# Kernel tuning notes

Hardware: AMD Instinct MI355X
Metric: run time of the kernel (lower is better)

Reference implementation:

```python
import jax, jax.numpy as jnp
import numpy as np

N_NODES = 100000
N_EDGES = 1600000
IN_DIM, HID_DIM, OUT_DIM = 256, 64, 64


def gcn_conv(x, src, dst, W, b, n_nodes):
    """PyG GCNConv: D^-1/2 (A + I) D^-1/2 X W + b (self-loops added, deg on dst)."""
    h = x @ W  # [N, D_out]
    ones = jnp.ones(src.shape[0], dtype=h.dtype)
    deg = jax.ops.segment_sum(ones, dst, num_segments=n_nodes) + 1.0  # +1 for self-loop
    dinv = jax.lax.rsqrt(deg)  # deg >= 1, always finite
    norm = dinv[src] * dinv[dst]  # [E]
    # neighbor aggregation (scatter-add) + self-loop contribution
    agg = jax.ops.segment_sum(h[src] * norm[:, None], dst, num_segments=n_nodes)
    agg = agg + h * (dinv * dinv)[:, None]
    return agg + b


def gcn_backbone(x, edge_index, W1, b1, W2, b2, n_nodes):
    src, dst = edge_index[0], edge_index[1]
    h = jax.nn.relu(gcn_conv(x, src, dst, W1, b1, n_nodes))
    h = gcn_conv(h, src, dst, W2, b2, n_nodes)
    return h


def zscore(h):
    # torch .std(0) is unbiased (ddof=1)
    return (h - h.mean(axis=0)) / jnp.std(h, axis=0, ddof=1)


def setup_inputs() -> dict:
    key = jax.random.key(0)
    k = jax.random.split(key, 8)
    x1 = jax.random.normal(k[0], (N_NODES, IN_DIM), dtype=jnp.float32)
    x2 = jax.random.normal(k[1], (N_NODES, IN_DIM), dtype=jnp.float32)
    edge_index1 = jax.random.randint(k[2], (2, N_EDGES), 0, N_NODES, dtype=jnp.int64)
    edge_index2 = jax.random.randint(k[3], (2, N_EDGES), 0, N_NODES, dtype=jnp.int64)
    W1 = jax.random.normal(k[4], (IN_DIM, HID_DIM), dtype=jnp.float32) * (1.0 / np.sqrt(IN_DIM))
    b1 = jnp.zeros((HID_DIM,), dtype=jnp.float32)
    W2 = jax.random.normal(k[5], (HID_DIM, OUT_DIM), dtype=jnp.float32) * (1.0 / np.sqrt(HID_DIM))
    b2 = jnp.zeros((OUT_DIM,), dtype=jnp.float32)
    return {"x1": x1, "edge_index1": edge_index1, "x2": x2, "edge_index2": edge_index2,
            "W1": W1, "b1": b1, "W2": W2, "b2": b2}


def reference(x1, edge_index1, x2, edge_index2, W1, b1, W2, b2):
    h1 = gcn_backbone(x1, edge_index1, W1, b1, W2, b2, N_NODES)
    h2 = gcn_backbone(x2, edge_index2, W1, b1, W2, b2, N_NODES)
    return zscore(h1), zscore(h2)
```

## Files before the change

### kernel.cpp

```cpp
#include <hip/hip_runtime.h>
#include <hip/hip_bf16.h>

#define HD 64
#define CH 8192
#define BKT_SHIFT 10
#define SRC_BITS 17
#define MAXBLK 256

typedef __attribute__((ext_vector_type(8))) short bf16x8;
typedef __attribute__((ext_vector_type(4))) float f32x4;

typedef __attribute__((address_space(1))) const unsigned int* gas_ptr;
typedef __attribute__((address_space(3))) unsigned int* las_ptr;

__device__ inline void gl_lds16(const void* g, void* l) {
  __builtin_amdgcn_global_load_lds((gas_ptr)g, (las_ptr)l, 16, 0, 0);
}

__device__ inline unsigned short f2bf(float x) {
  unsigned u = __float_as_uint(x);
  unsigned r = u + 0x7FFF + ((u >> 16) & 1);
  return (unsigned short)(r >> 16);
}
__device__ inline float bf2f(unsigned short h) {
  return __uint_as_float(((unsigned)h) << 16);
}

__global__ __launch_bounds__(256) void k_wprep(const float* __restrict__ W1,
                                               const float* __restrict__ W2,
                                               unsigned short* __restrict__ Wf1,
                                               unsigned short* __restrict__ Wf2hi,
                                               unsigned short* __restrict__ Wf2lo) {
  int idx = blockIdx.x * blockDim.x + threadIdx.x;
  if (idx < 256 * 64) {
    int k = idx >> 6, c = idx & 63;
    float w = W1[idx];
    int ks = k >> 5, r = k & 31, h2 = r >> 3, j = r & 7;
    int f = c >> 4, r16c = c & 15;
    int pos = (((ks * 4 + f) * 64) + h2 * 16 + r16c) * 8 + j;
    Wf1[pos] = f2bf(w);
  } else if (idx < 256 * 64 + 64 * 64) {
    int i2 = idx - 256 * 64;
    int k = i2 >> 6, c = i2 & 63;
    float w = W2[i2];
    int ks = k >> 5, r = k & 31, h2 = r >> 3, j = r & 7;
    int f = c >> 4, r16c = c & 15;
    int pos = (((ks * 4 + f) * 64) + h2 * 16 + r16c) * 8 + j;
    unsigned short hi = f2bf(w);
    Wf2hi[pos] = hi;
    Wf2lo[pos] = f2bf(w - bf2f(hi));
  }
}

__global__ __launch_bounds__(256) void k_bin1(const int* __restrict__ src0,
                                              const int* __restrict__ dst0,
                                              const int* __restrict__ src1,
                                              const int* __restrict__ dst1,
                                              int* __restrict__ tmp,
                                              int* __restrict__ counts,
                                              int* __restrict__ offsets,
                                              int NB, int NBLK, int E) {
  __shared__ int hist[128];
  __shared__ int pref[128];
  __shared__ int lofs[128];
  __shared__ int stage[CH];
  const int g = blockIdx.x / NBLK;
  const int blk = blockIdx.x % NBLK;
  const int* __restrict__ src = g ? src1 : src0;
  const int* __restrict__ dst = g ? dst1 : dst0;
  int* __restrict__ tmpg = tmp + (size_t)g * NBLK * CH;
  int* __restrict__ cntg = counts + (size_t)g * NB * NBLK;
  int* __restrict__ offg = offsets + (size_t)g * NB * NBLK;
  const int e0 = blk * CH;
  const int len = min(CH, E - e0);
  const int t = threadIdx.x;

  for (int i = t; i < 128; i += 256) hist[i] = 0;
  __syncthreads();
  int dreg[CH / 256];
#pragma unroll
  for (int it = 0; it < CH / 256; ++it) {
    int i = t + it * 256;
    if (i < len) {
      int d = dst[e0 + i];
      dreg[it] = d;
      atomicAdd(&hist[d >> BKT_SHIFT], 1);
    }
  }
  __syncthreads();
  if (t < 128) pref[t] = hist[t];
  __syncthreads();
  for (int off = 1; off < 128; off <<= 1) {
    int v = 0;
    if (t < 128 && t >= off) v = pref[t - off];
    __syncthreads();
    if (t < 128) pref[t] += v;
    __syncthreads();
  }
  if (t < NB) {
    int ex = pref[t] - hist[t];
    lofs[t] = ex;
    cntg[t * NBLK + blk] = hist[t];
    offg[t * NBLK + blk] = ex;
  }
  __syncthreads();
#pragma unroll
  for (int it = 0; it < CH / 256; ++it) {
    int i = t + it * 256;
    if (i < len) {
      int d = dreg[it], s = src[e0 + i];
      int slot = atomicAdd(&lofs[d >> BKT_SHIFT], 1);
      stage[slot] = ((d & ((1 << BKT_SHIFT) - 1)) << SRC_BITS) | s;
    }
  }
  __syncthreads();
  int nv = len >> 2;
  for (int i = t; i < nv; i += 256) ((int4*)(tmpg + e0))[i] = ((const int4*)stage)[i];
  for (int i = (nv << 2) + t; i < len; i += 256) tmpg[e0 + i] = stage[i];
}

__global__ __launch_bounds__(128) void k_bscan(const int* __restrict__ counts,
                                               int* __restrict__ bucket_base,
                                               int* __restrict__ row_start,
                                               int NB, int NBLK, int N, int E) {
  __shared__ int sh[128];
  const int g = blockIdx.x;
  const int* __restrict__ cntg = counts + (size_t)g * NB * NBLK;
  int* __restrict__ bbg = bucket_base + g * (NB + 1);
  int* __restrict__ rsg = row_start + (size_t)g * (N + 1);
  int t = threadIdx.x;
  int v = 0;
  if (t < NB) {
    const int* p = cntg + t * NBLK;
    for (int i = 0; i < NBLK; ++i) v += p[i];
  }
  sh[t] = v;
  __syncthreads();
  for (int off = 1; off < 128; off <<= 1) {
    int x = (t >= off) ? sh[t - off] : 0;
    __syncthreads();
    sh[t] += x;
    __syncthreads();
  }
  if (t < NB) bbg[t] = sh[t] - v;
  if (t == 0) {
    bbg[NB] = E;
    rsg[N] = E;
  }
}

__global__ __launch_bounds__(1024) void k_bin2m(const int* __restrict__ tmp,
                                                const int* __restrict__ counts,
                                                const int* __restrict__ offsets,
                                                const int* __restrict__ bucket_base,
                                                int* __restrict__ row_start,
                                                float* __restrict__ dinv,
                                                int* __restrict__ recs, int N, int NB,
                                                int NBLK, int E) {
  __shared__ int h[1 << BKT_SHIFT];
  __shared__ int lcur[1 << BKT_SHIFT];
  __shared__ int scnt[MAXBLK], soff[MAXBLK];
  const int g = blockIdx.x / NB;
  const int b = blockIdx.x % NB;
  const int* __restrict__ tmpg = tmp + (size_t)g * NBLK * CH;
  const int* __restrict__ cntg = counts + (size_t)g * NB * NBLK;
  const int* __restrict__ offg = offsets + (size_t)g * NB * NBLK;
  const int* __restrict__ bbg = bucket_base + g * (NB + 1);
  int* __restrict__ rsg = row_start + (size_t)g * (N + 1);
  float* __restrict__ dig = dinv + (size_t)g * N;
  int* __restrict__ recg = recs + (size_t)g * E;
  const int t = threadIdx.x;
  const int node0 = b << BKT_SHIFT;
  const int lane = t & 63, w = t >> 6;

  h[t] = 0;
  for (int i = t; i < NBLK; i += 1024) {
    scnt[i] = cntg[b * NBLK + i];
    soff[i] = offg[b * NBLK + i];
  }
  __syncthreads();
  for (int blk = w; blk < NBLK; blk += 16) {
    int cnt = scnt[blk];
    const int* p = tmpg + blk * CH + soff[blk];
    for (int j = lane; j < cnt; j += 64) atomicAdd(&h[p[j] >> SRC_BITS], 1);
  }
  __syncthreads();
  int deg = h[t];
  __syncthreads();
  for (int off = 1; off < 1024; off <<= 1) {
    int x = (t >= off) ? h[t - off] : 0;
    __syncthreads();
    h[t] += x;
    __syncthreads();
  }
  int base = bbg[b] + h[t] - deg;
  lcur[t] = base;
  int n = node0 + t;
  if (n < N) {
    rsg[n] = base;
    dig[n] = rsqrtf((float)deg + 1.0f);
  }
  __syncthreads();
  for (int blk = w; blk < NBLK; blk += 16) {
    int cnt = scnt[blk];
    const int* p = tmpg + blk * CH + soff[blk];
    for (int j = lane; j < cnt; j += 64) {
      int rec = p[j];
      int d = rec >> SRC_BITS;
      int s = rec & ((1 << SRC_BITS) - 1);
      int slot = atomicAdd(&lcur[d], 1);
      recg[slot] = s;
    }
  }
}

__global__ __launch_bounds__(256) void k_gemm1(const float* __restrict__ X0,
                                               const float* __restrict__ X1,
                                               const unsigned short* __restrict__ Wf1,
                                               unsigned short* __restrict__ Hb, int N,
                                               int gPer) {
  __shared__ float sA[2][64 * 64];
  const int tid = threadIdx.x;
  const int g = blockIdx.x / gPer;
  const int bblk = blockIdx.x % gPer;
  const float* __restrict__ Xv = g ? X1 : X0;
  const int row0 = bblk * 64;
  const int lane = tid & 63;
  const int wv = tid >> 6;
  const int r16 = lane & 15;
  const int half = lane >> 4;
  const int rowL = wv * 16 + r16;

  auto STAGE = [&](int b, int c) {
#pragma unroll
    for (int i = 0; i < 4; ++i) {
      int slot = tid + i * 256;
      int r = slot >> 4, u = slot & 15;
      int su = (u & 8) | ((u & 7) ^ (r & 7));
      int gr = min(row0 + r, N - 1);
      gl_lds16(Xv + (size_t)gr * 256 + c * 64 + su * 4, (char*)&sA[b][0] + slot * 16);
    }
  };

  f32x4 acc[4];
#pragma unroll
  for (int f = 0; f < 4; ++f) acc[f] = (f32x4){0.f, 0.f, 0.f, 0.f};

  STAGE(0, 0);
  for (int c = 0; c < 4; ++c) {
    const int buf = c & 1;
    if (c < 3) STAGE(buf ^ 1, c + 1);
    __syncthreads();
#pragma unroll
    for (int ks2 = 0; ks2 < 2; ++ks2) {
      const int ksg = c * 2 + ks2;
      int v0 = ks2 * 8 + half * 2;
      int p0 = (v0 & 8) | ((v0 & 7) ^ (rowL & 7));
      int p1 = ((v0 + 1) & 8) | (((v0 + 1) & 7) ^ (rowL & 7));
      float4 a0 = *(const float4*)((const char*)&sA[buf][0] + (rowL * 16 + p0) * 16);
      float4 a1 = *(const float4*)((const char*)&sA[buf][0] + (rowL * 16 + p1) * 16);
      union { __hip_bfloat162 h[4]; bf16x8 v; } cu;
      cu.h[0] = __float22bfloat162_rn(make_float2(a0.x, a0.y));
      cu.h[1] = __float22bfloat162_rn(make_float2(a0.z, a0.w));
      cu.h[2] = __float22bfloat162_rn(make_float2(a1.x, a1.y));
      cu.h[3] = __float22bfloat162_rn(make_float2(a1.z, a1.w));
      bf16x8 ahi = cu.v;
#pragma unroll
      for (int f = 0; f < 4; ++f) {
        bf16x8 bh = *(const bf16x8*)&Wf1[(((ksg * 4 + f) * 64) + lane) * 8];
        acc[f] = __builtin_amdgcn_mfma_f32_16x16x32_bf16(ahi, bh, acc[f], 0, 0, 0);
      }
    }
    __syncthreads();
  }

  const int orow0 = row0 + wv * 16 + half * 4;
#pragma unroll
  for (int f = 0; f < 4; ++f) {
#pragma unroll
    for (int rg = 0; rg < 4; ++rg) {
      int orow = orow0 + rg;
      if (orow < N) Hb[((size_t)g * N + orow) * HD + f * 16 + r16] = f2bf(acc[f][rg]);
    }
  }
}

__global__ __launch_bounds__(256) void k_gemm2(const unsigned short* __restrict__ Xb,
                                               const unsigned short* __restrict__ Wfh,
                                               const unsigned short* __restrict__ Wfl,
                                               unsigned short* __restrict__ Hb, int M) {
  __shared__ unsigned short sA[64 * 64];
  const int tid = threadIdx.x;
  const int row0 = blockIdx.x * 64;
  const int lane = tid & 63;
  const int wv = tid >> 6;
  const int r16 = lane & 15;
  const int half = lane >> 4;
  const int rowL = wv * 16 + r16;

#pragma unroll
  for (int i = 0; i < 2; ++i) {
    int slot = tid + i * 256;
    int r = slot >> 3, u = slot & 7;
    int su = u ^ (r & 7);
    int gr = min(row0 + r, M - 1);
    gl_lds16(Xb + (size_t)gr * 64 + su * 8, (char*)sA + slot * 16);
  }
  __syncthreads();

  f32x4 acc[4];
#pragma unroll
  for (int f = 0; f < 4; ++f) acc[f] = (f32x4){0.f, 0.f, 0.f, 0.f};

#pragma unroll
  for (int ks = 0; ks < 2; ++ks) {
    int v = ks * 4 + half;
    int p = v ^ (rowL & 7);
    bf16x8 ahi = *(const bf16x8*)((const char*)sA + (rowL * 8 + p) * 16);
#pragma unroll
    for (int f = 0; f < 4; ++f) {
      bf16x8 bh = *(const bf16x8*)&Wfh[(((ks * 4 + f) * 64) + lane) * 8];
      bf16x8 bl = *(const bf16x8*)&Wfl[(((ks * 4 + f) * 64) + lane) * 8];
      acc[f] = __builtin_amdgcn_mfma_f32_16x16x32_bf16(ahi, bh, acc[f], 0, 0, 0);
      acc[f] = __builtin_amdgcn_mfma_f32_16x16x32_bf16(ahi, bl, acc[f], 0, 0, 0);
    }
  }

  const int orow0 = row0 + wv * 16 + half * 4;
#pragma unroll
  for (int f = 0; f < 4; ++f) {
#pragma unroll
    for (int rg = 0; rg < 4; ++rg) {
      int orow = orow0 + rg;
      if (orow < M) Hb[(size_t)orow * HD + f * 16 + r16] = f2bf(acc[f][rg]);
    }
  }
}

template <int OUTBF16>
__global__ __launch_bounds__(256) void k_agg(const unsigned short* __restrict__ Hb,
                                             const int* __restrict__ recs,
                                             const int* __restrict__ row_start,
                                             const float* __restrict__ dinv,
                                             const float* __restrict__ bias,
                                             void* __restrict__ outv, int N, int E,
                                             int relu) {
  const int t = threadIdx.x;
  const int nglob = (blockIdx.x * blockDim.x + t) >> 4;
  const int lane16 = t & 15;
  if (nglob >= 2 * N) return;
  const int g = nglob >= N;
  const int node = nglob - g * N;
  const int* __restrict__ rsg = row_start + (size_t)g * (N + 1);
  const int* __restrict__ R = recs + (size_t)g * E;
  const float* __restrict__ dig = dinv + (size_t)g * N;
  const unsigned short* __restrict__ Hbg = Hb + (size_t)g * N * HD;

  const int c0 = lane16 * 4;
  float di = dig[node];
  float a0, a1, a2, a3;
  {
    uint2 h = *(const uint2*)&Hbg[(size_t)node * HD + c0];
    float dd = di * di;
    a0 = bf2f((unsigned short)(h.x & 0xffff)) * dd;
    a1 = bf2f((unsigned short)(h.x >> 16)) * dd;
    a2 = bf2f((unsigned short)(h.y & 0xffff)) * dd;
    a3 = bf2f((unsigned short)(h.y >> 16)) * dd;
  }
  const int beg = rsg[node], end = rsg[node + 1];
  int e = beg;
  for (; e + 8 <= end; e += 8) {
    int s[8];
    uint2 gg[8];
    float n[8];
#pragma unroll
    for (int j = 0; j < 8; ++j) s[j] = R[e + j];
#pragma unroll
    for (int j = 0; j < 8; ++j) {
      gg[j] = *(const uint2*)&Hbg[(size_t)s[j] * HD + c0];
      n[j] = dig[s[j]];
    }
#pragma unroll
    for (int j = 0; j < 8; ++j) {
      float nn = n[j] * di;
      a0 = fmaf(bf2f((unsigned short)(gg[j].x & 0xffff)), nn, a0);
      a1 = fmaf(bf2f((unsigned short)(gg[j].x >> 16)), nn, a1);
      a2 = fmaf(bf2f((unsigned short)(gg[j].y & 0xffff)), nn, a2);
      a3 = fmaf(bf2f((unsigned short)(gg[j].y >> 16)), nn, a3);
    }
  }
  for (; e < end; ++e) {
    int s = R[e];
    uint2 gg = *(const uint2*)&Hbg[(size_t)s * HD + c0];
    float nn = dig[s] * di;
    a0 = fmaf(bf2f((unsigned short)(gg.x & 0xffff)), nn, a0);
    a1 = fmaf(bf2f((unsigned short)(gg.x >> 16)), nn, a1);
    a2 = fmaf(bf2f((unsigned short)(gg.y & 0xffff)), nn, a2);
    a3 = fmaf(bf2f((unsigned short)(gg.y >> 16)), nn, a3);
  }
  float4 bv = *(const float4*)&bias[c0];
  a0 += bv.x; a1 += bv.y; a2 += bv.z; a3 += bv.w;
  if (relu) {
    a0 = fmaxf(a0, 0.f); a1 = fmaxf(a1, 0.f);
    a2 = fmaxf(a2, 0.f); a3 = fmaxf(a3, 0.f);
  }
  if (OUTBF16) {
    uint2 o;
    o.x = ((unsigned)f2bf(a1) << 16) | f2bf(a0);
    o.y = ((unsigned)f2bf(a3) << 16) | f2bf(a2);
    *(uint2*)&((unsigned short*)outv)[(size_t)nglob * HD + c0] = o;
  } else {
    *(float4*)&((float*)outv)[(size_t)nglob * HD + c0] = make_float4(a0, a1, a2, a3);
  }
}


__global__ void k_colstats(const float* __restrict__ H, float* __restrict__ stats, int N,
                           int gridPer) {
  __shared__ float ss[256], sq[256];
  const int g = blockIdx.x / gridPer;
  const int blk = blockIdx.x % gridPer;
  const float* __restrict__ Hg = H + (size_t)g * N * HD;
  float* __restrict__ st = stats + g * 128;
  int t = threadIdx.x;
  int col = t & 63, grp = t >> 6;
  float s = 0.f, q = 0.f;
  for (int row = blk * 4 + grp; row < N; row += gridPer * 4) {
    float v = Hg[(size_t)row * HD + col];
    s += v;
    q += v * v;
  }
  ss[t] = s;
  sq[t] = q;
  __syncthreads();
  if (t < 64) {
    s = ss[t] + ss[t + 64] + ss[t + 128] + ss[t + 192];
    q = sq[t] + sq[t + 64] + sq[t + 128] + sq[t + 192];
    atomicAdd(&st[t], s);
    atomicAdd(&st[64 + t], q);
  }
}

__global__ void k_normalize(float* __restrict__ H, const float* __restrict__ stats, int N) {
  int i = blockIdx.x * blockDim.x + threadIdx.x;
  int total = 2 * N * HD;
  if (i >= total) return;
  int col = i & 63;
  const float* st = stats + (i >= N * HD ? 128 : 0);
  float sum = st[col], sumsq = st[64 + col];
  float mean = sum / (float)N;
  float var = (sumsq - sum * sum / (float)N) / (float)(N - 1);
  float r = rsqrtf(var);
  H[i] = (H[i] - mean) * r;
}


extern "C" void kernel_launch(void* const* d_in, const int* in_sizes, int n_in,
                              void* d_out, int out_size, void* d_ws, size_t ws_size,
                              hipStream_t stream) {
  const int IN_DIM = 256;
  const float* X1 = (const float*)d_in[0];
  const float* X2 = (const float*)d_in[2];
  const int* EI1 = (const int*)d_in[1];
  const int* EI2 = (const int*)d_in[3];
  const float* W1 = (const float*)d_in[4];
  const float* b1 = (const float*)d_in[5];
  const float* W2 = (const float*)d_in[6];
  const float* b2 = (const float*)d_in[7];
  const int N = in_sizes[0] / IN_DIM;
  const int E = in_sizes[1] / 2;
  const int NB = (N + (1 << BKT_SHIFT) - 1) >> BKT_SHIFT;
  const int NBLK = (E + CH - 1) / CH;

  char* ws = (char*)d_ws;
  size_t off = 0;
  auto carve = [&](size_t bytes) -> char* {
    char* p = ws + off;
    off += (bytes + 255) & ~(size_t)255;
    return p;
  };
  unsigned short* Hb = (unsigned short*)carve((size_t)2 * N * HD * 2);
  int* tmp = (int*)carve((size_t)2 * NBLK * CH * 4);
  int* recs = (int*)carve((size_t)2 * E * 4);
  char* zero_base = carve(256 * 4);
  float* stats = (float*)zero_base;
  int* row_start = (int*)carve((size_t)2 * (N + 1) * 4);
  float* dinv = (float*)carve((size_t)2 * N * 4);
  int* bucket_base = (int*)carve((size_t)2 * (NB + 1) * 4);
  int* counts = (int*)carve((size_t)2 * NB * NBLK * 4);
  int* offsets = (int*)carve((size_t)2 * NB * NBLK * 4);
  unsigned short* Wf1 = (unsigned short*)carve(256 * 64 * 2);
  unsigned short* Wf2hi = (unsigned short*)carve(64 * 64 * 2);
  unsigned short* Wf2lo = (unsigned short*)carve(64 * 64 * 2);
  unsigned short* bufAgg = (unsigned short*)d_out;
  (void)ws_size; (void)n_in; (void)out_size;

  const int T = 256;
  const int gPer1 = (N + 63) / 64;
  const int gG2 = (2 * N + 63) / 64;
  const int gAgg = (2 * N * 16 + T - 1) / T;
  const int gCS = 512;
  const int gElem = (2 * N * HD + T - 1) / T;
  const int gWp = (256 * 64 + 64 * 64 + T - 1) / T;

  (void)hipMemsetAsync(zero_base, 0, 256 * 4, stream);
  k_wprep<<<gWp, T, 0, stream>>>(W1, W2, Wf1, Wf2hi, Wf2lo);
  k_bin1<<<2 * NBLK, T, 0, stream>>>(EI1, EI1 + E, EI2, EI2 + E, tmp, counts, offsets,
                                     NB, NBLK, E);
  k_bscan<<<2, 128, 0, stream>>>(counts, bucket_base, row_start, NB, NBLK, N, E);
  k_bin2m<<<2 * NB, 1024, 0, stream>>>(tmp, counts, offsets, bucket_base, row_start,
                                       dinv, recs, N, NB, NBLK, E);

  k_gemm1<<<2 * gPer1, T, 0, stream>>>(X1, X2, Wf1, Hb, N, gPer1);
  k_agg<1><<<gAgg, T, 0, stream>>>(Hb, recs, row_start, dinv, b1, bufAgg, N, E, 1);
  k_gemm2<<<gG2, T, 0, stream>>>(bufAgg, Wf2hi, Wf2lo, Hb, 2 * N);
  k_agg<0><<<gAgg, T, 0, stream>>>(Hb, recs, row_start, dinv, b2, d_out, N, E, 0);

  k_colstats<<<2 * gCS, T, 0, stream>>>((float*)d_out, stats, N, gCS);
  k_normalize<<<gElem, T, 0, stream>>>((float*)d_out, stats, N);
}
```

Before: 363.9 us.

## Load GEMM operands directly into registers via inline asm, dropping LDS staging

Both dense GEMM kernels stop staging the activation tile through shared memory with global_load_lds and barriers. Each lane now issues its own dwordx4 global loads straight into registers from inline assembly, covering its A-fragment rows and all the weight fragments, then waits with explicit vmcnt waits. In gemm1 the second half of the weights is loaded while the first half of the MFMAs runs. This removes LDS traffic and __syncthreads, but raises register pressure (many vector registers held per lane) and bypasses the compiler's own scheduling of the loads.

```diff
diff --git a/kernel.cpp b/kernel.cpp
--- a/kernel.cpp
+++ b/kernel.cpp
@@ -9,13 +9,10 @@
 
 typedef __attribute__((ext_vector_type(8))) short bf16x8;
 typedef __attribute__((ext_vector_type(4))) float f32x4;
-
-typedef __attribute__((address_space(1))) const unsigned int* gas_ptr;
-typedef __attribute__((address_space(3))) unsigned int* las_ptr;
-
-__device__ inline void gl_lds16(const void* g, void* l) {
-  __builtin_amdgcn_global_load_lds((gas_ptr)g, (las_ptr)l, 16, 0, 0);
-}
+typedef __attribute__((ext_vector_type(4))) unsigned int u32x4;
+
+#define WAITALL do { asm volatile("s_waitcnt vmcnt(0)" ::: "memory"); \
+                     __builtin_amdgcn_sched_barrier(0); } while (0)
 
 __device__ inline unsigned short f2bf(float x) {
   unsigned u = __float_as_uint(x);
@@ -219,62 +216,124 @@
                                                const unsigned short* __restrict__ Wf1,
                                                unsigned short* __restrict__ Hb, int N,
                                                int gPer) {
-  __shared__ float sA[2][64 * 64];
   const int tid = threadIdx.x;
   const int g = blockIdx.x / gPer;
   const int bblk = blockIdx.x % gPer;
   const float* __restrict__ Xv = g ? X1 : X0;
-  const int row0 = bblk * 64;
   const int lane = tid & 63;
   const int wv = tid >> 6;
   const int r16 = lane & 15;
   const int half = lane >> 4;
-  const int rowL = wv * 16 + r16;
-
-  auto STAGE = [&](int b, int c) {
-#pragma unroll
-    for (int i = 0; i < 4; ++i) {
-      int slot = tid + i * 256;
-      int r = slot >> 4, u = slot & 15;
-      int su = (u & 8) | ((u & 7) ^ (r & 7));
-      int gr = min(row0 + r, N - 1);
-      gl_lds16(Xv + (size_t)gr * 256 + c * 64 + su * 4, (char*)&sA[b][0] + slot * 16);
-    }
-  };
+  const int row = bblk * 64 + wv * 16 + r16;
+  const int rowc = min(row, N - 1);
+
+  unsigned long long xa =
+      (unsigned long long)(const void*)(Xv + (size_t)rowc * 256 + half * 8);
+  f32x4 a[16];
+  asm volatile(
+      "global_load_dwordx4 %0, %16, off\n\t"
+      "global_load_dwordx4 %1, %16, off offset:16\n\t"
+      "global_load_dwordx4 %2, %16, off offset:128\n\t"
+      "global_load_dwordx4 %3, %16, off offset:144\n\t"
+      "global_load_dwordx4 %4, %16, off offset:256\n\t"
+      "global_load_dwordx4 %5, %16, off offset:272\n\t"
+      "global_load_dwordx4 %6, %16, off offset:384\n\t"
+      "global_load_dwordx4 %7, %16, off offset:400\n\t"
+      "global_load_dwordx4 %8, %16, off offset:512\n\t"
+      "global_load_dwordx4 %9, %16, off offset:528\n\t"
+      "global_load_dwordx4 %10, %16, off offset:640\n\t"
+      "global_load_dwordx4 %11, %16, off offset:656\n\t"
+      "global_load_dwordx4 %12, %16, off offset:768\n\t"
+      "global_load_dwordx4 %13, %16, off offset:784\n\t"
+      "global_load_dwordx4 %14, %16, off offset:896\n\t"
+      "global_load_dwordx4 %15, %16, off offset:912\n\t"
+      : "=&v"(a[0]), "=&v"(a[1]), "=&v"(a[2]), "=&v"(a[3]), "=&v"(a[4]),
+        "=&v"(a[5]), "=&v"(a[6]), "=&v"(a[7]), "=&v"(a[8]), "=&v"(a[9]),
+        "=&v"(a[10]), "=&v"(a[11]), "=&v"(a[12]), "=&v"(a[13]), "=&v"(a[14]),
+        "=&v"(a[15])
+      : "v"(xa));
+
+  const unsigned long long wb = (unsigned long long)(const void*)Wf1 + lane * 16;
+  bf16x8 B[32];
+  asm volatile(
+      "global_load_dwordx4 %0, %16, off\n\t"
+      "global_load_dwordx4 %1, %16, off offset:1024\n\t"
+      "global_load_dwordx4 %2, %16, off offset:2048\n\t"
+      "global_load_dwordx4 %3, %16, off offset:3072\n\t"
+      "global_load_dwordx4 %4, %17, off\n\t"
+      "global_load_dwordx4 %5, %17, off offset:1024\n\t"
+      "global_load_dwordx4 %6, %17, off offset:2048\n\t"
+      "global_load_dwordx4 %7, %17, off offset:3072\n\t"
+      "global_load_dwordx4 %8, %18, off\n\t"
+      "global_load_dwordx4 %9, %18, off offset:1024\n\t"
+      "global_load_dwordx4 %10, %18, off offset:2048\n\t"
+      "global_load_dwordx4 %11, %18, off offset:3072\n\t"
+      "global_load_dwordx4 %12, %19, off\n\t"
+      "global_load_dwordx4 %13, %19, off offset:1024\n\t"
+      "global_load_dwordx4 %14, %19, off offset:2048\n\t"
+      "global_load_dwordx4 %15, %19, off offset:3072\n\t"
+      : "=&v"(B[0]), "=&v"(B[1]), "=&v"(B[2]), "=&v"(B[3]), "=&v"(B[4]),
+        "=&v"(B[5]), "=&v"(B[6]), "=&v"(B[7]), "=&v"(B[8]), "=&v"(B[9]),
+        "=&v"(B[10]), "=&v"(B[11]), "=&v"(B[12]), "=&v"(B[13]), "=&v"(B[14]),
+        "=&v"(B[15])
+      : "v"(wb), "v"(wb + 4096), "v"(wb + 8192), "v"(wb + 12288));
+
+  WAITALL;
+
+  asm volatile(
+      "global_load_dwordx4 %0, %16, off\n\t"
+      "global_load_dwordx4 %1, %16, off offset:1024\n\t"
+      "global_load_dwordx4 %2, %16, off offset:2048\n\t"
+      "global_load_dwordx4 %3, %16, off offset:3072\n\t"
+      "global_load_dwordx4 %4, %17, off\n\t"
+      "global_load_dwordx4 %5, %17, off offset:1024\n\t"
+      "global_load_dwordx4 %6, %17, off offset:2048\n\t"
+      "global_load_dwordx4 %7, %17, off offset:3072\n\t"
+      "global_load_dwordx4 %8, %18, off\n\t"
+      "global_load_dwordx4 %9, %18, off offset:1024\n\t"
+      "global_load_dwordx4 %10, %18, off offset:2048\n\t"
+      "global_load_dwordx4 %11, %18, off offset:3072\n\t"
+      "global_load_dwordx4 %12, %19, off\n\t"
+      "global_load_dwordx4 %13, %19, off offset:1024\n\t"
+      "global_load_dwordx4 %14, %19, off offset:2048\n\t"
+      "global_load_dwordx4 %15, %19, off offset:3072\n\t"
+      : "=&v"(B[16]), "=&v"(B[17]), "=&v"(B[18]), "=&v"(B[19]), "=&v"(B[20]),
+        "=&v"(B[21]), "=&v"(B[22]), "=&v"(B[23]), "=&v"(B[24]), "=&v"(B[25]),
+        "=&v"(B[26]), "=&v"(B[27]), "=&v"(B[28]), "=&v"(B[29]), "=&v"(B[30]),
+        "=&v"(B[31])
+      : "v"(wb + 16384), "v"(wb + 20480), "v"(wb + 24576), "v"(wb + 28672));
 
   f32x4 acc[4];
 #pragma unroll
   for (int f = 0; f < 4; ++f) acc[f] = (f32x4){0.f, 0.f, 0.f, 0.f};
 
-  STAGE(0, 0);
-  for (int c = 0; c < 4; ++c) {
-    const int buf = c & 1;
-    if (c < 3) STAGE(buf ^ 1, c + 1);
-    __syncthreads();
-#pragma unroll
-    for (int ks2 = 0; ks2 < 2; ++ks2) {
-      const int ksg = c * 2 + ks2;
-      int v0 = ks2 * 8 + half * 2;
-      int p0 = (v0 & 8) | ((v0 & 7) ^ (rowL & 7));
-      int p1 = ((v0 + 1) & 8) | (((v0 + 1) & 7) ^ (rowL & 7));
-      float4 a0 = *(const float4*)((const char*)&sA[buf][0] + (rowL * 16 + p0) * 16);
-      float4 a1 = *(const float4*)((const char*)&sA[buf][0] + (rowL * 16 + p1) * 16);
-      union { __hip_bfloat162 h[4]; bf16x8 v; } cu;
-      cu.h[0] = __float22bfloat162_rn(make_float2(a0.x, a0.y));
-      cu.h[1] = __float22bfloat162_rn(make_float2(a0.z, a0.w));
-      cu.h[2] = __float22bfloat162_rn(make_float2(a1.x, a1.y));
-      cu.h[3] = __float22bfloat162_rn(make_float2(a1.z, a1.w));
-      bf16x8 ahi = cu.v;
-#pragma unroll
-      for (int f = 0; f < 4; ++f) {
-        bf16x8 bh = *(const bf16x8*)&Wf1[(((ksg * 4 + f) * 64) + lane) * 8];
-        acc[f] = __builtin_amdgcn_mfma_f32_16x16x32_bf16(ahi, bh, acc[f], 0, 0, 0);
-      }
-    }
-    __syncthreads();
-  }
-
-  const int orow0 = row0 + wv * 16 + half * 4;
+#pragma unroll
+  for (int ks = 0; ks < 4; ++ks) {
+    union { __hip_bfloat162 h[4]; bf16x8 v; } cu;
+    cu.h[0] = __float22bfloat162_rn(make_float2(a[2 * ks][0], a[2 * ks][1]));
+    cu.h[1] = __float22bfloat162_rn(make_float2(a[2 * ks][2], a[2 * ks][3]));
+    cu.h[2] = __float22bfloat162_rn(make_float2(a[2 * ks + 1][0], a[2 * ks + 1][1]));
+    cu.h[3] = __float22bfloat162_rn(make_float2(a[2 * ks + 1][2], a[2 * ks + 1][3]));
+#pragma unroll
+    for (int f = 0; f < 4; ++f)
+      acc[f] = __builtin_amdgcn_mfma_f32_16x16x32_bf16(cu.v, B[ks * 4 + f], acc[f], 0, 0, 0);
+  }
+
+  WAITALL;
+
+#pragma unroll
+  for (int ks = 4; ks < 8; ++ks) {
+    union { __hip_bfloat162 h[4]; bf16x8 v; } cu;
+    cu.h[0] = __float22bfloat162_rn(make_float2(a[2 * ks][0], a[2 * ks][1]));
+    cu.h[1] = __float22bfloat162_rn(make_float2(a[2 * ks][2], a[2 * ks][3]));
+    cu.h[2] = __float22bfloat162_rn(make_float2(a[2 * ks + 1][0], a[2 * ks + 1][1]));
+    cu.h[3] = __float22bfloat162_rn(make_float2(a[2 * ks + 1][2], a[2 * ks + 1][3]));
+#pragma unroll
+    for (int f = 0; f < 4; ++f)
+      acc[f] = __builtin_amdgcn_mfma_f32_16x16x32_bf16(cu.v, B[ks * 4 + f], acc[f], 0, 0, 0);
+  }
+
+  const int orow0 = bblk * 64 + wv * 16 + half * 4;
 #pragma unroll
   for (int f = 0; f < 4; ++f) {
 #pragma unroll
@@ -289,41 +348,61 @@
                                                const unsigned short* __restrict__ Wfh,
                                                const unsigned short* __restrict__ Wfl,
                                                unsigned short* __restrict__ Hb, int M) {
-  __shared__ unsigned short sA[64 * 64];
   const int tid = threadIdx.x;
   const int row0 = blockIdx.x * 64;
   const int lane = tid & 63;
   const int wv = tid >> 6;
   const int r16 = lane & 15;
   const int half = lane >> 4;
-  const int rowL = wv * 16 + r16;
-
-#pragma unroll
-  for (int i = 0; i < 2; ++i) {
-    int slot = tid + i * 256;
-    int r = slot >> 3, u = slot & 7;
-    int su = u ^ (r & 7);
-    int gr = min(row0 + r, M - 1);
-    gl_lds16(Xb + (size_t)gr * 64 + su * 8, (char*)sA + slot * 16);
-  }
-  __syncthreads();
+  const int row = row0 + wv * 16 + r16;
+  const int rowc = min(row, M - 1);
+
+  unsigned long long xa =
+      (unsigned long long)(const void*)(Xb + (size_t)rowc * 64 + half * 8);
+  const unsigned long long bh = (unsigned long long)(const void*)Wfh + lane * 16;
+  const unsigned long long bl = (unsigned long long)(const void*)Wfl + lane * 16;
+  u32x4 A0, A1;
+  bf16x8 BH[8], BL[8];
+  asm volatile(
+      "global_load_dwordx4 %0, %18, off\n\t"
+      "global_load_dwordx4 %1, %18, off offset:64\n\t"
+      "global_load_dwordx4 %2, %19, off\n\t"
+      "global_load_dwordx4 %3, %19, off offset:1024\n\t"
+      "global_load_dwordx4 %4, %19, off offset:2048\n\t"
+      "global_load_dwordx4 %5, %19, off offset:3072\n\t"
+      "global_load_dwordx4 %6, %20, off\n\t"
+      "global_load_dwordx4 %7, %20, off offset:1024\n\t"
+      "global_load_dwordx4 %8, %20, off offset:2048\n\t"
+      "global_load_dwordx4 %9, %20, off offset:3072\n\t"
+      "global_load_dwordx4 %10, %21, off\n\t"
+      "global_load_dwordx4 %11, %21, off offset:1024\n\t"
+      "global_load_dwordx4 %12, %21, off offset:2048\n\t"
+      "global_load_dwordx4 %13, %21, off offset:3072\n\t"
+      "global_load_dwordx4 %14, %22, off\n\t"
+      "global_load_dwordx4 %15, %22, off offset:1024\n\t"
+      "global_load_dwordx4 %16, %22, off offset:2048\n\t"
+      "global_load_dwordx4 %17, %22, off offset:3072\n\t"
+      : "=&v"(A0), "=&v"(A1), "=&v"(BH[0]), "=&v"(BH[1]), "=&v"(BH[2]),
+        "=&v"(BH[3]), "=&v"(BH[4]), "=&v"(BH[5]), "=&v"(BH[6]), "=&v"(BH[7]),
+        "=&v"(BL[0]), "=&v"(BL[1]), "=&v"(BL[2]), "=&v"(BL[3]), "=&v"(BL[4]),
+        "=&v"(BL[5]), "=&v"(BL[6]), "=&v"(BL[7])
+      : "v"(xa), "v"(bh), "v"(bh + 4096), "v"(bl), "v"(bl + 4096));
+
+  WAITALL;
 
   f32x4 acc[4];
 #pragma unroll
   for (int f = 0; f < 4; ++f) acc[f] = (f32x4){0.f, 0.f, 0.f, 0.f};
 
-#pragma unroll
-  for (int ks = 0; ks < 2; ++ks) {
-    int v = ks * 4 + half;
-    int p = v ^ (rowL & 7);
-    bf16x8 ahi = *(const bf16x8*)((const char*)sA + (rowL * 8 + p) * 16);
-#pragma unroll
-    for (int f = 0; f < 4; ++f) {
-      bf16x8 bh = *(const bf16x8*)&Wfh[(((ks * 4 + f) * 64) + lane) * 8];
-      bf16x8 bl = *(const bf16x8*)&Wfl[(((ks * 4 + f) * 64) + lane) * 8];
-      acc[f] = __builtin_amdgcn_mfma_f32_16x16x32_bf16(ahi, bh, acc[f], 0, 0, 0);
-      acc[f] = __builtin_amdgcn_mfma_f32_16x16x32_bf16(ahi, bl, acc[f], 0, 0, 0);
-    }
+  union { u32x4 u; bf16x8 v; } a0u, a1u;
+  a0u.u = A0;
+  a1u.u = A1;
+#pragma unroll
+  for (int f = 0; f < 4; ++f) {
+    acc[f] = __builtin_amdgcn_mfma_f32_16x16x32_bf16(a0u.v, BH[f], acc[f], 0, 0, 0);
+    acc[f] = __builtin_amdgcn_mfma_f32_16x16x32_bf16(a0u.v, BL[f], acc[f], 0, 0, 0);
+    acc[f] = __builtin_amdgcn_mfma_f32_16x16x32_bf16(a1u.v, BH[4 + f], acc[f], 0, 0, 0);
+    acc[f] = __builtin_amdgcn_mfma_f32_16x16x32_bf16(a1u.v, BL[4 + f], acc[f], 0, 0, 0);
   }
 
   const int orow0 = row0 + wv * 16 + half * 4;
```

Result: no change. 369.5 us (+1.5%).
